# Performance work log

Hardware: AMD Instinct MI355X
Metric: run time of the kernel (lower is better)

The kernel has to match this reference:

```python
import jax, jax.numpy as jnp
import numpy as np

EPS = 1e-5

def _ln(x, g, b):
    mu = jnp.mean(x, axis=-1, keepdims=True)
    var = jnp.mean((x - mu) ** 2, axis=-1, keepdims=True)
    return (x - mu) * jax.lax.rsqrt(var + EPS) * g + b

def setup_inputs() -> dict:
    key = jax.random.key(0)
    ks = jax.random.split(key, 12)
    B, T, D, H = 8, 2048, 64, 8
    hs = D // H  # 8
    s = 0.05
    return {
        'x': jax.random.normal(ks[0], (B, T, D), dtype=jnp.float32),
        # per-head Q/K/V weights stacked: [H, hs, D] (torch Linear weight layout [out, in])
        'Wq': jax.random.normal(ks[1], (H, hs, D), dtype=jnp.float32) * s,
        'Wk': jax.random.normal(ks[2], (H, hs, D), dtype=jnp.float32) * s,
        'Wv': jax.random.normal(ks[3], (H, hs, D), dtype=jnp.float32) * s,
        'Wproj': jax.random.normal(ks[4], (D, H * hs), dtype=jnp.float32) * s,
        'bproj': jnp.zeros((D,), dtype=jnp.float32),
        'W1': jax.random.normal(ks[5], (4 * D, D), dtype=jnp.float32) * s,
        'b1': jnp.zeros((4 * D,), dtype=jnp.float32),
        'W2': jax.random.normal(ks[6], (D, 4 * D), dtype=jnp.float32) * s,
        'b2': jnp.zeros((D,), dtype=jnp.float32),
        'ln1_g': jnp.ones((D,), dtype=jnp.float32),
        'ln1_b': jnp.zeros((D,), dtype=jnp.float32),
        'ln2_g': jnp.ones((D,), dtype=jnp.float32),
        'ln2_b': jnp.zeros((D,), dtype=jnp.float32),
    }

def reference(x, Wq, Wk, Wv, Wproj, bproj, W1, b1, W2, b2, ln1_g, ln1_b, ln2_g, ln2_b):
    # pre-LN self-attention (dropout = identity, eval mode)
    h = _ln(x, ln1_g, ln1_b)
    q = jnp.einsum('btd,hsd->bhts', h, Wq)  # [B,H,T,hs]
    k = jnp.einsum('btd,hsd->bhts', h, Wk)
    v = jnp.einsum('btd,hsd->bhts', h, Wv)
    scale = Wk.shape[1] ** -0.5  # k.shape[-1]**-0.5 in original
    wei = jax.nn.softmax(jnp.einsum('bhts,bhus->bhtu', q, k) * scale, axis=-1)
    o = jnp.einsum('bhtu,bhus->bhts', wei, v)  # [B,H,T,hs]
    B, H, T, hs = o.shape
    o = o.transpose(0, 2, 1, 3).reshape(B, T, H * hs)  # concat heads
    x = x + o @ Wproj.T + bproj
    # pre-LN MLP
    h2 = _ln(x, ln2_g, ln2_b)
    ff = jax.nn.relu(h2 @ W1.T + b1) @ W2.T + b2
    return x + ff
```

## Files before the change

### kernel.cpp

```cpp
#include <hip/hip_runtime.h>
#include <hip/hip_fp16.h>

#define DEV static __device__ __forceinline__

constexpr int NTOK = 8 * 2048;
constexpr float LN_EPS = 1e-5f;

using half4  = __attribute__((ext_vector_type(4))) _Float16;
using half8  = __attribute__((ext_vector_type(8))) _Float16;
using f32x4  = __attribute__((ext_vector_type(4))) float;
using f32x16 = __attribute__((ext_vector_type(16))) float;

DEV __half2 bch2(unsigned u) { return __builtin_bit_cast(__half2, u); }
DEV unsigned bcu(__half2 h)  { return __builtin_bit_cast(unsigned, h); }

#define MFMA16(a, b, c)    __builtin_amdgcn_mfma_f32_16x16x16f16(a, b, c, 0, 0, 0)
#define MFMA32(a, b, c)    __builtin_amdgcn_mfma_f32_32x32x8f16(a, b, c, 0, 0, 0)
#define MFMA32X16(a, b, c) __builtin_amdgcn_mfma_f32_32x32x16_f16(a, b, c, 0, 0, 0)

DEV half4 pk4(float a, float b, float c, float d) {
  unsigned lo = __builtin_bit_cast(unsigned, __builtin_amdgcn_cvt_pkrtz(a, b));
  unsigned hi = __builtin_bit_cast(unsigned, __builtin_amdgcn_cvt_pkrtz(c, d));
  uint2 u = make_uint2(lo, hi);
  return __builtin_bit_cast(half4, u);
}
DEV half8 cat8(uint2 a, uint2 b) {
  uint4 u = make_uint4(a.x, a.y, b.x, b.y);
  return __builtin_bit_cast(half8, u);
}
DEV half8 cat8h(half4 a, half4 b) {
  return cat8(__builtin_bit_cast(uint2, a), __builtin_bit_cast(uint2, b));
}

DEV float schr(float x) {
  return __builtin_bit_cast(float, (int)__builtin_fmaf(x, 8388608.0f, 1064987473.0f));
}

__global__ __launch_bounds__(256) void k_ln_qkv(
    const float* __restrict__ x, const float* __restrict__ Wq,
    const float* __restrict__ Wk, const float* __restrict__ Wv,
    const float* __restrict__ g1, const float* __restrict__ b1g,
    __half* __restrict__ Qo, __half* __restrict__ Ko, __half* __restrict__ Vo)
{
  __shared__ __align__(16) __half WqF[4096];
  __shared__ __align__(16) __half WkF[4096];
  __shared__ __align__(16) __half WvF[4096];
  const int tid = threadIdx.x, lane = tid & 63, wid = tid >> 6;
  const int l15 = lane & 15, gg = lane >> 4;
  const float qs = 0.35355339059327373f * 1.4426950408889634f;
  for (int idx = tid; idx < 1024; idx += 256) {
    int mt = idx >> 8, kt = (idx >> 6) & 3, l = idx & 63;
    int row = l & 15, g = l >> 4;
    int off = (mt * 16 + row) * 64 + kt * 16 + g * 4;
    float4 a = *(const float4*)(Wq + off);
    float4 b = *(const float4*)(Wk + off);
    float4 c = *(const float4*)(Wv + off);
    half4 hq; hq[0] = (_Float16)(a.x*qs); hq[1] = (_Float16)(a.y*qs);
    hq[2] = (_Float16)(a.z*qs); hq[3] = (_Float16)(a.w*qs);
    half4 hk; hk[0] = (_Float16)b.x; hk[1] = (_Float16)b.y;
    hk[2] = (_Float16)b.z; hk[3] = (_Float16)b.w;
    half4 hv; hv[0] = (_Float16)c.x; hv[1] = (_Float16)c.y;
    hv[2] = (_Float16)c.z; hv[3] = (_Float16)c.w;
    *(half4*)&WqF[idx * 4] = hq;
    *(half4*)&WkF[idx * 4] = hk;
    *(half4*)&WvF[idx * 4] = hv;
  }
  __syncthreads();

  const int tok = (blockIdx.x * 4 + wid) * 16 + l15;
  const int b = tok >> 11, t = tok & 2047;
  float4 xv[4];
  float sum = 0.f, sq = 0.f;
  #pragma unroll
  for (int kt = 0; kt < 4; ++kt) {
    xv[kt] = *(const float4*)(x + tok * 64 + kt * 16 + gg * 4);
    sum += xv[kt].x + xv[kt].y + xv[kt].z + xv[kt].w;
    sq  += xv[kt].x*xv[kt].x + xv[kt].y*xv[kt].y
         + xv[kt].z*xv[kt].z + xv[kt].w*xv[kt].w;
  }
  sum += __shfl_xor(sum, 16); sum += __shfl_xor(sum, 32);
  sq  += __shfl_xor(sq, 16);  sq  += __shfl_xor(sq, 32);
  float mu = sum * (1.0f / 64.0f);
  float var = sq * (1.0f / 64.0f) - mu * mu;
  float rs = rsqrtf(var + LN_EPS);
  half4 hb[4];
  #pragma unroll
  for (int kt = 0; kt < 4; ++kt) {
    float4 gv = *(const float4*)(g1 + kt * 16 + gg * 4);
    float4 bv = *(const float4*)(b1g + kt * 16 + gg * 4);
    hb[kt][0] = (_Float16)((xv[kt].x - mu) * rs * gv.x + bv.x);
    hb[kt][1] = (_Float16)((xv[kt].y - mu) * rs * gv.y + bv.y);
    hb[kt][2] = (_Float16)((xv[kt].z - mu) * rs * gv.z + bv.z);
    hb[kt][3] = (_Float16)((xv[kt].w - mu) * rs * gv.w + bv.w);
  }
  #pragma unroll
  for (int mt = 0; mt < 4; ++mt) {
    f32x4 oq = {}, ok = {}, ov = {};
    #pragma unroll
    for (int kt = 0; kt < 4; ++kt) {
      half4 q_a = *(const half4*)&WqF[((mt * 4 + kt) * 64 + lane) * 4];
      half4 k_a = *(const half4*)&WkF[((mt * 4 + kt) * 64 + lane) * 4];
      half4 v_a = *(const half4*)&WvF[((mt * 4 + kt) * 64 + lane) * 4];
      oq = MFMA16(q_a, hb[kt], oq);
      ok = MFMA16(k_a, hb[kt], ok);
      ov = MFMA16(v_a, hb[kt], ov);
    }
    const int sg = mt * 16 + gg * 4;
    const int h = sg >> 3, s = sg & 7;
    const long base = ((long)(b * 8 + h) * 2048 + t) * 8 + s;
    *(half4*)(Qo + base) = pk4(oq[0], oq[1], oq[2], oq[3]);
    *(half4*)(Ko + base) = pk4(ok[0], ok[1], ok[2], ok[3]);
    *(half4*)(Vo + base) = pk4(ov[0], ov[1], ov[2], ov[3]);
  }
}

__global__ __launch_bounds__(256, 4) void k_attn(
    const __half* __restrict__ Qg, const __half* __restrict__ Kg,
    const __half* __restrict__ Vg, __half* __restrict__ Og)
{
  __shared__ __align__(16) char VTs[9 * 4128];
  const int tid = threadIdx.x, lane = tid & 63, wid = tid >> 6;
  const int bh = blockIdx.x;
  const int base = bh << 14;
  const uint4* Vu = (const uint4*)(Vg + base);
  for (int i = tid; i < 1024; i += 256) {
    uint4 a = Vu[2 * i], bq = Vu[2 * i + 1];
    const unsigned short* pa = (const unsigned short*)&a;
    const unsigned short* pb = (const unsigned short*)&bq;
    #pragma unroll
    for (int d = 0; d < 8; ++d) {
      unsigned val = (unsigned)pa[d] | ((unsigned)pb[d] << 16);
      *(unsigned*)(VTs + d * 4128 + i * 4) = val;
    }
    *(unsigned*)(VTs + 8 * 4128 + i * 4) = 0x3C003C00u;
  }
  __syncthreads();

  const int b = bh >> 3, hh = bh & 7;
  const int l31 = lane & 31, hi = lane >> 5;
  const int q0 = blockIdx.y * 256 + wid * 64;
  half4 qf0 = *(const half4*)((const char*)(Qg + base) + (q0 + l31) * 16 + hi * 8);
  half4 qf1 = *(const half4*)((const char*)(Qg + base) + (q0 + 32 + l31) * 16 + hi * 8);
  const char* kp = (const char*)(Kg + base) + l31 * 16 + hi * 8;
  const int deff = (l31 <= 8) ? l31 : 8;
  const char* vb = VTs + deff * 4128 + hi * 8;

  const f32x16 z = {};
  f32x16 o0 = {}, o1 = {};
  half4 kA[8], kB[8];
  #pragma unroll
  for (int u = 0; u < 8; ++u) kA[u] = *(const half4*)(kp + u * 512);

  #define ATTN_BODY(KF, VB, IMM)                                               \
    {                                                                          \
      f32x16 s0 = MFMA32(KF, qf0, z);                                          \
      f32x16 s1 = MFMA32(KF, qf1, z);                                          \
      uint2 vl0 = *(const uint2*)((VB) + (IMM));                               \
      uint2 vh0 = *(const uint2*)((VB) + (IMM) + 16);                          \
      uint2 vl1 = *(const uint2*)((VB) + (IMM) + 32);                          \
      uint2 vh1 = *(const uint2*)((VB) + (IMM) + 48);                          \
      half4 pa0 = pk4(schr(s0[0]),  schr(s0[1]),  schr(s0[2]),  schr(s0[3]));  \
      half4 pa1 = pk4(schr(s0[4]),  schr(s0[5]),  schr(s0[6]),  schr(s0[7]));  \
      o0 = MFMA32X16(cat8(vl0, vh0), cat8h(pa0, pa1), o0);                     \
      half4 pb0 = pk4(schr(s1[0]),  schr(s1[1]),  schr(s1[2]),  schr(s1[3]));  \
      half4 pb1 = pk4(schr(s1[4]),  schr(s1[5]),  schr(s1[6]),  schr(s1[7]));  \
      o1 = MFMA32X16(cat8(vl0, vh0), cat8h(pb0, pb1), o1);                     \
      half4 pa2 = pk4(schr(s0[8]),  schr(s0[9]),  schr(s0[10]), schr(s0[11])); \
      half4 pa3 = pk4(schr(s0[12]), schr(s0[13]), schr(s0[14]), schr(s0[15])); \
      o0 = MFMA32X16(cat8(vl1, vh1), cat8h(pa2, pa3), o0);                     \
      half4 pb2 = pk4(schr(s1[8]),  schr(s1[9]),  schr(s1[10]), schr(s1[11])); \
      half4 pb3 = pk4(schr(s1[12]), schr(s1[13]), schr(s1[14]), schr(s1[15])); \
      o1 = MFMA32X16(cat8(vl1, vh1), cat8h(pb2, pb3), o1);                     \
    }

  #pragma unroll 1
  for (int gp = 0; gp < 4; ++gp) {
    const char* vbg = vb + gp * 1024;
    const char* kpe = kp + gp * 8192;
    #pragma unroll
    for (int u = 0; u < 8; ++u) kB[u] = *(const half4*)(kpe + 4096 + u * 512);
    #pragma unroll
    for (int u = 0; u < 8; ++u) ATTN_BODY(kA[u], vbg, u * 64);
    if (gp < 3) {
      #pragma unroll
      for (int u = 0; u < 8; ++u) kA[u] = *(const half4*)(kpe + 8192 + u * 512);
    }
    #pragma unroll
    for (int u = 0; u < 8; ++u) ATTN_BODY(kB[u], vbg, 512 + u * 64);
  }
  #undef ATTN_BODY

  {
    float l0 = __shfl(o0[4], l31);
    float inv = 1.0f / l0;
    half4 r;
    r[0] = (_Float16)(o0[0] * inv); r[1] = (_Float16)(o0[1] * inv);
    r[2] = (_Float16)(o0[2] * inv); r[3] = (_Float16)(o0[3] * inv);
    *(half4*)(Og + ((b * 2048 + q0 + l31) * 64) + hh * 8 + hi * 4) = r;
  }
  {
    float l1 = __shfl(o1[4], l31);
    float inv = 1.0f / l1;
    half4 r;
    r[0] = (_Float16)(o1[0] * inv); r[1] = (_Float16)(o1[1] * inv);
    r[2] = (_Float16)(o1[2] * inv); r[3] = (_Float16)(o1[3] * inv);
    *(half4*)(Og + ((b * 2048 + q0 + 32 + l31) * 64) + hh * 8 + hi * 4) = r;
  }
}

__global__ __launch_bounds__(256) void k_proj_mlp(
    const float* __restrict__ x, const __half* __restrict__ Og,
    const float* __restrict__ Wproj, const float* __restrict__ bproj,
    const float* __restrict__ W1, const float* __restrict__ b1,
    const float* __restrict__ W2, const float* __restrict__ b2,
    const float* __restrict__ g2, const float* __restrict__ bb2,
    float* __restrict__ out)
{
  __shared__ __align__(16) __half WpF[4096];
  __shared__ __align__(16) __half W1F[16384];
  __shared__ __align__(16) __half W2F[16384];
  __shared__ __align__(16) float biasLDS[512];
  const int tid = threadIdx.x, lane = tid & 63, wid = tid >> 6;
  const int l15 = lane & 15, gg = lane >> 4;

  for (int idx = tid; idx < 1024; idx += 256) {
    int mt = idx >> 8, kt = (idx >> 6) & 3, l = idx & 63;
    int row = l & 15, g = l >> 4;
    float4 w = *(const float4*)(Wproj + (mt * 16 + row) * 64 + kt * 16 + g * 4);
    half4 h; h[0] = (_Float16)w.x; h[1] = (_Float16)w.y;
    h[2] = (_Float16)w.z; h[3] = (_Float16)w.w;
    *(half4*)&WpF[idx * 4] = h;
  }
  for (int idx = tid; idx < 4096; idx += 256) {
    int mt2 = idx >> 8, kt = (idx >> 6) & 3, l = idx & 63;
    int row = l & 15, g = l >> 4;
    float4 w = *(const float4*)(W1 + (mt2 * 16 + row) * 64 + kt * 16 + g * 4);
    half4 h; h[0] = (_Float16)w.x; h[1] = (_Float16)w.y;
    h[2] = (_Float16)w.z; h[3] = (_Float16)w.w;
    *(half4*)&W1F[idx * 4] = h;
  }
  for (int idx = tid; idx < 4096; idx += 256) {
    int mt = idx >> 10, kt2 = (idx >> 6) & 15, l = idx & 63;
    int row = l & 15, g = l >> 4;
    float4 w = *(const float4*)(W2 + (mt * 16 + row) * 256 + kt2 * 16 + g * 4);
    half4 h; h[0] = (_Float16)w.x; h[1] = (_Float16)w.y;
    h[2] = (_Float16)w.z; h[3] = (_Float16)w.w;
    *(half4*)&W2F[idx * 4] = h;
  }
  for (int idx = tid; idx < 512; idx += 256) {
    float v;
    if      (idx <  64) v = bproj[idx];
    else if (idx < 128) v = g2[idx - 64];
    else if (idx < 192) v = bb2[idx - 128];
    else if (idx < 256) v = b2[idx - 192];
    else                v = b1[idx - 256];
    biasLDS[idx] = v;
  }
  __syncthreads();

  const int tile = blockIdx.x * 4 + wid;
  const int tok = tile * 16 + l15;

  const __half* orow = Og + tok * 64;
  half4 ob[4];
  #pragma unroll
  for (int kt = 0; kt < 4; ++kt)
    ob[kt] = __builtin_bit_cast(half4, *(const uint2*)(orow + kt * 16 + gg * 4));

  f32x4 acc[4];
  #pragma unroll
  for (int mt = 0; mt < 4; ++mt) {
    float4 xv = *(const float4*)(x + tok * 64 + mt * 16 + gg * 4);
    float4 bp = *(const float4*)&biasLDS[mt * 16 + gg * 4];
    acc[mt] = (f32x4){xv.x + bp.x, xv.y + bp.y, xv.z + bp.z, xv.w + bp.w};
    #pragma unroll
    for (int kt = 0; kt < 4; ++kt) {
      half4 wa = *(const half4*)&WpF[((mt * 4 + kt) * 64 + lane) * 4];
      acc[mt] = MFMA16(wa, ob[kt], acc[mt]);
    }
  }
  float sum = 0.f, sq = 0.f;
  #pragma unroll
  for (int mt = 0; mt < 4; ++mt) {
    #pragma unroll
    for (int r = 0; r < 4; ++r) { float v = acc[mt][r]; sum += v; sq += v * v; }
  }
  sum += __shfl_xor(sum, 16); sum += __shfl_xor(sum, 32);
  sq  += __shfl_xor(sq, 16);  sq  += __shfl_xor(sq, 32);
  float mu = sum * (1.0f / 64.0f);
  float var = sq * (1.0f / 64.0f) - mu * mu;
  float rs = rsqrtf(var + LN_EPS);
  half4 hb[4];
  #pragma unroll
  for (int mt = 0; mt < 4; ++mt) {
    float4 gv = *(const float4*)&biasLDS[64 + mt * 16 + gg * 4];
    float4 bv = *(const float4*)&biasLDS[128 + mt * 16 + gg * 4];
    hb[mt][0] = (_Float16)((acc[mt][0] - mu) * rs * gv.x + bv.x);
    hb[mt][1] = (_Float16)((acc[mt][1] - mu) * rs * gv.y + bv.y);
    hb[mt][2] = (_Float16)((acc[mt][2] - mu) * rs * gv.z + bv.z);
    hb[mt][3] = (_Float16)((acc[mt][3] - mu) * rs * gv.w + bv.w);
  }
  half4 pf[16];
  #pragma unroll
  for (int mt2 = 0; mt2 < 16; ++mt2) {
    float4 b1v = *(const float4*)&biasLDS[256 + mt2 * 16 + gg * 4];
    f32x4 f = (f32x4){b1v.x, b1v.y, b1v.z, b1v.w};
    #pragma unroll
    for (int kt = 0; kt < 4; ++kt) {
      half4 wa = *(const half4*)&W1F[((mt2 * 4 + kt) * 64 + lane) * 4];
      f = MFMA16(wa, hb[kt], f);
    }
    pf[mt2][0] = (_Float16)fmaxf(f[0], 0.f);
    pf[mt2][1] = (_Float16)fmaxf(f[1], 0.f);
    pf[mt2][2] = (_Float16)fmaxf(f[2], 0.f);
    pf[mt2][3] = (_Float16)fmaxf(f[3], 0.f);
  }
  #pragma unroll
  for (int mt = 0; mt < 4; ++mt) {
    float4 b2v = *(const float4*)&biasLDS[192 + mt * 16 + gg * 4];
    f32x4 o = (f32x4){acc[mt][0] + b2v.x, acc[mt][1] + b2v.y,
                      acc[mt][2] + b2v.z, acc[mt][3] + b2v.w};
    #pragma unroll
    for (int kt2 = 0; kt2 < 16; ++kt2) {
      half4 wa = *(const half4*)&W2F[((mt * 16 + kt2) * 64 + lane) * 4];
      o = MFMA16(wa, pf[kt2], o);
    }
    *(float4*)(out + tok * 64 + mt * 16 + gg * 4) =
        make_float4(o[0], o[1], o[2], o[3]);
  }
}

extern "C" void kernel_launch(void* const* d_in, const int* in_sizes, int n_in,
                              void* d_out, int out_size, void* d_ws, size_t ws_size,
                              hipStream_t stream) {
  const float* x     = (const float*)d_in[0];
  const float* Wq    = (const float*)d_in[1];
  const float* Wk    = (const float*)d_in[2];
  const float* Wv    = (const float*)d_in[3];
  const float* Wproj = (const float*)d_in[4];
  const float* bproj = (const float*)d_in[5];
  const float* W1    = (const float*)d_in[6];
  const float* b1    = (const float*)d_in[7];
  const float* W2    = (const float*)d_in[8];
  const float* b2    = (const float*)d_in[9];
  const float* g1    = (const float*)d_in[10];
  const float* bb1   = (const float*)d_in[11];
  const float* g2    = (const float*)d_in[12];
  const float* bb2   = (const float*)d_in[13];
  float* out = (float*)d_out;

  __half* Qh = (__half*)d_ws;
  __half* Kh = Qh + 1048576;
  __half* Vh = Kh + 1048576;
  __half* Oc = Vh + 1048576;

  k_ln_qkv<<<256, 256, 0, stream>>>(x, Wq, Wk, Wv, g1, bb1, Qh, Kh, Vh);
  k_attn<<<dim3(64, 8), 256, 0, stream>>>(Qh, Kh, Vh, Oc);
  k_proj_mlp<<<256, 256, 0, stream>>>(x, Oc, Wproj, bproj, W1, b1, W2, b2,
                                      g2, bb2, out);
}
```

Baseline: 50.69 us.

## Fold Schraudolph exp scaling into weights and software-pipeline QK MFMAs

```diff
diff --git a/kernel.cpp b/kernel.cpp
--- a/kernel.cpp
+++ b/kernel.cpp
@@ -31,10 +31,7 @@
 DEV half8 cat8h(half4 a, half4 b) {
   return cat8(__builtin_bit_cast(uint2, a), __builtin_bit_cast(uint2, b));
 }
-
-DEV float schr(float x) {
-  return __builtin_bit_cast(float, (int)__builtin_fmaf(x, 8388608.0f, 1064987473.0f));
-}
+DEV float ib(float x) { return __builtin_bit_cast(float, (int)x); }
 
 __global__ __launch_bounds__(256) void k_ln_qkv(
     const float* __restrict__ x, const float* __restrict__ Wq,
@@ -47,7 +44,8 @@
   __shared__ __align__(16) __half WvF[4096];
   const int tid = threadIdx.x, lane = tid & 63, wid = tid >> 6;
   const int l15 = lane & 15, gg = lane >> 4;
-  const float qs = 0.35355339059327373f * 1.4426950408889634f;
+  const float qs = 0.35355339059327373f * 1.4426950408889634f * 2048.0f;
+  const float ks = 4096.0f;
   for (int idx = tid; idx < 1024; idx += 256) {
     int mt = idx >> 8, kt = (idx >> 6) & 3, l = idx & 63;
     int row = l & 15, g = l >> 4;
@@ -57,8 +55,8 @@
     float4 c = *(const float4*)(Wv + off);
     half4 hq; hq[0] = (_Float16)(a.x*qs); hq[1] = (_Float16)(a.y*qs);
     hq[2] = (_Float16)(a.z*qs); hq[3] = (_Float16)(a.w*qs);
-    half4 hk; hk[0] = (_Float16)b.x; hk[1] = (_Float16)b.y;
-    hk[2] = (_Float16)b.z; hk[3] = (_Float16)b.w;
+    half4 hk; hk[0] = (_Float16)(b.x*ks); hk[1] = (_Float16)(b.y*ks);
+    hk[2] = (_Float16)(b.z*ks); hk[3] = (_Float16)(b.w*ks);
     half4 hv; hv[0] = (_Float16)c.x; hv[1] = (_Float16)c.y;
     hv[2] = (_Float16)c.z; hv[3] = (_Float16)c.w;
     *(half4*)&WqF[idx * 4] = hq;
@@ -114,7 +112,7 @@
   }
 }
 
-__global__ __launch_bounds__(256, 4) void k_attn(
+__global__ __launch_bounds__(256, 2) void k_attn(
     const __half* __restrict__ Qg, const __half* __restrict__ Kg,
     const __half* __restrict__ Vg, __half* __restrict__ Og)
 {
@@ -145,33 +143,37 @@
   const int deff = (l31 <= 8) ? l31 : 8;
   const char* vb = VTs + deff * 4128 + hi * 8;
 
-  const f32x16 z = {};
-  f32x16 o0 = {}, o1 = {};
+  f32x16 cm;
+  #pragma unroll
+  for (int i = 0; i < 16; ++i) cm[i] = 1064987473.0f;
+
+  f32x16 o0l = {}, o0h = {}, o1l = {}, o1h = {};
   half4 kA[8], kB[8];
   #pragma unroll
   for (int u = 0; u < 8; ++u) kA[u] = *(const half4*)(kp + u * 512);
 
-  #define ATTN_BODY(KF, VB, IMM)                                               \
+  #define PVB(SC0, SC1, VB, IMM)                                               \
     {                                                                          \
-      f32x16 s0 = MFMA32(KF, qf0, z);                                          \
-      f32x16 s1 = MFMA32(KF, qf1, z);                                          \
       uint2 vl0 = *(const uint2*)((VB) + (IMM));                               \
       uint2 vh0 = *(const uint2*)((VB) + (IMM) + 16);                          \
       uint2 vl1 = *(const uint2*)((VB) + (IMM) + 32);                          \
       uint2 vh1 = *(const uint2*)((VB) + (IMM) + 48);                          \
-      half4 pa0 = pk4(schr(s0[0]),  schr(s0[1]),  schr(s0[2]),  schr(s0[3]));  \
-      half4 pa1 = pk4(schr(s0[4]),  schr(s0[5]),  schr(s0[6]),  schr(s0[7]));  \
-      o0 = MFMA32X16(cat8(vl0, vh0), cat8h(pa0, pa1), o0);                     \
-      half4 pb0 = pk4(schr(s1[0]),  schr(s1[1]),  schr(s1[2]),  schr(s1[3]));  \
-      half4 pb1 = pk4(schr(s1[4]),  schr(s1[5]),  schr(s1[6]),  schr(s1[7]));  \
-      o1 = MFMA32X16(cat8(vl0, vh0), cat8h(pb0, pb1), o1);                     \
-      half4 pa2 = pk4(schr(s0[8]),  schr(s0[9]),  schr(s0[10]), schr(s0[11])); \
-      half4 pa3 = pk4(schr(s0[12]), schr(s0[13]), schr(s0[14]), schr(s0[15])); \
-      o0 = MFMA32X16(cat8(vl1, vh1), cat8h(pa2, pa3), o0);                     \
-      half4 pb2 = pk4(schr(s1[8]),  schr(s1[9]),  schr(s1[10]), schr(s1[11])); \
-      half4 pb3 = pk4(schr(s1[12]), schr(s1[13]), schr(s1[14]), schr(s1[15])); \
-      o1 = MFMA32X16(cat8(vl1, vh1), cat8h(pb2, pb3), o1);                     \
-    }
+      half4 pa0 = pk4(ib(SC0[0]),  ib(SC0[1]),  ib(SC0[2]),  ib(SC0[3]));      \
+      half4 pa1 = pk4(ib(SC0[4]),  ib(SC0[5]),  ib(SC0[6]),  ib(SC0[7]));      \
+      o0l = MFMA32X16(cat8(vl0, vh0), cat8h(pa0, pa1), o0l);                   \
+      half4 pb0 = pk4(ib(SC1[0]),  ib(SC1[1]),  ib(SC1[2]),  ib(SC1[3]));      \
+      half4 pb1 = pk4(ib(SC1[4]),  ib(SC1[5]),  ib(SC1[6]),  ib(SC1[7]));      \
+      o1l = MFMA32X16(cat8(vl0, vh0), cat8h(pb0, pb1), o1l);                   \
+      half4 pa2 = pk4(ib(SC0[8]),  ib(SC0[9]),  ib(SC0[10]), ib(SC0[11]));     \
+      half4 pa3 = pk4(ib(SC0[12]), ib(SC0[13]), ib(SC0[14]), ib(SC0[15]));     \
+      o0h = MFMA32X16(cat8(vl1, vh1), cat8h(pa2, pa3), o0h);                   \
+      half4 pb2 = pk4(ib(SC1[8]),  ib(SC1[9]),  ib(SC1[10]), ib(SC1[11]));     \
+      half4 pb3 = pk4(ib(SC1[12]), ib(SC1[13]), ib(SC1[14]), ib(SC1[15]));     \
+      o1h = MFMA32X16(cat8(vl1, vh1), cat8h(pb2, pb3), o1h);                   \
+    }
+
+  f32x16 sc0 = MFMA32(kA[0], qf0, cm);
+  f32x16 sc1 = MFMA32(kA[0], qf1, cm);
 
   #pragma unroll 1
   for (int gp = 0; gp < 4; ++gp) {
@@ -180,17 +182,30 @@
     #pragma unroll
     for (int u = 0; u < 8; ++u) kB[u] = *(const half4*)(kpe + 4096 + u * 512);
     #pragma unroll
-    for (int u = 0; u < 8; ++u) ATTN_BODY(kA[u], vbg, u * 64);
+    for (int u = 0; u < 8; ++u) {
+      half4 kn = (u < 7) ? kA[u + 1] : kB[0];
+      f32x16 sn0 = MFMA32(kn, qf0, cm);
+      f32x16 sn1 = MFMA32(kn, qf1, cm);
+      PVB(sc0, sc1, vbg, u * 64);
+      sc0 = sn0; sc1 = sn1;
+    }
     if (gp < 3) {
       #pragma unroll
       for (int u = 0; u < 8; ++u) kA[u] = *(const half4*)(kpe + 8192 + u * 512);
     }
     #pragma unroll
-    for (int u = 0; u < 8; ++u) ATTN_BODY(kB[u], vbg, 512 + u * 64);
-  }
-  #undef ATTN_BODY
+    for (int u = 0; u < 8; ++u) {
+      half4 kn = (u < 7) ? kB[u + 1] : kA[0];
+      f32x16 sn0 = MFMA32(kn, qf0, cm);
+      f32x16 sn1 = MFMA32(kn, qf1, cm);
+      PVB(sc0, sc1, vbg, 512 + u * 64);
+      sc0 = sn0; sc1 = sn1;
+    }
+  }
+  #undef PVB
 
   {
+    f32x16 o0 = o0l + o0h;
     float l0 = __shfl(o0[4], l31);
     float inv = 1.0f / l0;
     half4 r;
@@ -199,6 +214,7 @@
     *(half4*)(Og + ((b * 2048 + q0 + l31) * 64) + hh * 8 + hi * 4) = r;
   }
   {
+    f32x16 o1 = o1l + o1h;
     float l1 = __shfl(o1[4], l31);
     float inv = 1.0f / l1;
     half4 r;
```

After: 46.45 us, median of 2. 1.09x faster.

## Split attention keys across two wave groups and fold the exp constant into MFMA accumulators

Applied to the files above, without the earlier changes.

```diff
diff --git a/kernel.cpp b/kernel.cpp
--- a/kernel.cpp
+++ b/kernel.cpp
@@ -31,10 +31,7 @@
 DEV half8 cat8h(half4 a, half4 b) {
   return cat8(__builtin_bit_cast(uint2, a), __builtin_bit_cast(uint2, b));
 }
-
-DEV float schr(float x) {
-  return __builtin_bit_cast(float, (int)__builtin_fmaf(x, 8388608.0f, 1064987473.0f));
-}
+DEV float ib(float x) { return __builtin_bit_cast(float, (int)x); }
 
 __global__ __launch_bounds__(256) void k_ln_qkv(
     const float* __restrict__ x, const float* __restrict__ Wq,
@@ -47,7 +44,8 @@
   __shared__ __align__(16) __half WvF[4096];
   const int tid = threadIdx.x, lane = tid & 63, wid = tid >> 6;
   const int l15 = lane & 15, gg = lane >> 4;
-  const float qs = 0.35355339059327373f * 1.4426950408889634f;
+  const float qs = 0.35355339059327373f * 1.4426950408889634f * 2048.0f;
+  const float ks = 4096.0f;
   for (int idx = tid; idx < 1024; idx += 256) {
     int mt = idx >> 8, kt = (idx >> 6) & 3, l = idx & 63;
     int row = l & 15, g = l >> 4;
@@ -57,8 +55,8 @@
     float4 c = *(const float4*)(Wv + off);
     half4 hq; hq[0] = (_Float16)(a.x*qs); hq[1] = (_Float16)(a.y*qs);
     hq[2] = (_Float16)(a.z*qs); hq[3] = (_Float16)(a.w*qs);
-    half4 hk; hk[0] = (_Float16)b.x; hk[1] = (_Float16)b.y;
-    hk[2] = (_Float16)b.z; hk[3] = (_Float16)b.w;
+    half4 hk; hk[0] = (_Float16)(b.x*ks); hk[1] = (_Float16)(b.y*ks);
+    hk[2] = (_Float16)(b.z*ks); hk[3] = (_Float16)(b.w*ks);
     half4 hv; hv[0] = (_Float16)c.x; hv[1] = (_Float16)c.y;
     hv[2] = (_Float16)c.z; hv[3] = (_Float16)c.w;
     *(half4*)&WqF[idx * 4] = hq;
@@ -114,16 +112,17 @@
   }
 }
 
-__global__ __launch_bounds__(256, 4) void k_attn(
+__global__ __launch_bounds__(512, 4) void k_attn(
     const __half* __restrict__ Qg, const __half* __restrict__ Kg,
     const __half* __restrict__ Vg, __half* __restrict__ Og)
 {
   __shared__ __align__(16) char VTs[9 * 4128];
+  __shared__ float Lc[4][2][64][5];
   const int tid = threadIdx.x, lane = tid & 63, wid = tid >> 6;
   const int bh = blockIdx.x;
   const int base = bh << 14;
   const uint4* Vu = (const uint4*)(Vg + base);
-  for (int i = tid; i < 1024; i += 256) {
+  for (int i = tid; i < 1024; i += 512) {
     uint4 a = Vu[2 * i], bq = Vu[2 * i + 1];
     const unsigned short* pa = (const unsigned short*)&a;
     const unsigned short* pb = (const unsigned short*)&bq;
@@ -138,14 +137,18 @@
 
   const int b = bh >> 3, hh = bh & 7;
   const int l31 = lane & 31, hi = lane >> 5;
-  const int q0 = blockIdx.y * 256 + wid * 64;
+  const int qt = wid & 3, kh = wid >> 2;
+  const int q0 = blockIdx.y * 256 + qt * 64;
   half4 qf0 = *(const half4*)((const char*)(Qg + base) + (q0 + l31) * 16 + hi * 8);
   half4 qf1 = *(const half4*)((const char*)(Qg + base) + (q0 + 32 + l31) * 16 + hi * 8);
-  const char* kp = (const char*)(Kg + base) + l31 * 16 + hi * 8;
+  const char* kp = (const char*)(Kg + base) + (kh << 14) + l31 * 16 + hi * 8;
   const int deff = (l31 <= 8) ? l31 : 8;
-  const char* vb = VTs + deff * 4128 + hi * 8;
-
-  const f32x16 z = {};
+  const char* vb = VTs + deff * 4128 + hi * 8 + kh * 2048;
+
+  f32x16 cm;
+  #pragma unroll
+  for (int i = 0; i < 16; ++i) cm[i] = 1064987473.0f;
+
   f32x16 o0 = {}, o1 = {};
   half4 kA[8], kB[8];
   #pragma unroll
@@ -153,35 +156,35 @@
 
   #define ATTN_BODY(KF, VB, IMM)                                               \
     {                                                                          \
-      f32x16 s0 = MFMA32(KF, qf0, z);                                          \
-      f32x16 s1 = MFMA32(KF, qf1, z);                                          \
+      f32x16 s0 = MFMA32(KF, qf0, cm);                                         \
+      f32x16 s1 = MFMA32(KF, qf1, cm);                                         \
       uint2 vl0 = *(const uint2*)((VB) + (IMM));                               \
       uint2 vh0 = *(const uint2*)((VB) + (IMM) + 16);                          \
       uint2 vl1 = *(const uint2*)((VB) + (IMM) + 32);                          \
       uint2 vh1 = *(const uint2*)((VB) + (IMM) + 48);                          \
-      half4 pa0 = pk4(schr(s0[0]),  schr(s0[1]),  schr(s0[2]),  schr(s0[3]));  \
-      half4 pa1 = pk4(schr(s0[4]),  schr(s0[5]),  schr(s0[6]),  schr(s0[7]));  \
+      half4 pa0 = pk4(ib(s0[0]),  ib(s0[1]),  ib(s0[2]),  ib(s0[3]));          \
+      half4 pa1 = pk4(ib(s0[4]),  ib(s0[5]),  ib(s0[6]),  ib(s0[7]));          \
       o0 = MFMA32X16(cat8(vl0, vh0), cat8h(pa0, pa1), o0);                     \
-      half4 pb0 = pk4(schr(s1[0]),  schr(s1[1]),  schr(s1[2]),  schr(s1[3]));  \
-      half4 pb1 = pk4(schr(s1[4]),  schr(s1[5]),  schr(s1[6]),  schr(s1[7]));  \
+      half4 pb0 = pk4(ib(s1[0]),  ib(s1[1]),  ib(s1[2]),  ib(s1[3]));          \
+      half4 pb1 = pk4(ib(s1[4]),  ib(s1[5]),  ib(s1[6]),  ib(s1[7]));          \
       o1 = MFMA32X16(cat8(vl0, vh0), cat8h(pb0, pb1), o1);                     \
-      half4 pa2 = pk4(schr(s0[8]),  schr(s0[9]),  schr(s0[10]), schr(s0[11])); \
-      half4 pa3 = pk4(schr(s0[12]), schr(s0[13]), schr(s0[14]), schr(s0[15])); \
+      half4 pa2 = pk4(ib(s0[8]),  ib(s0[9]),  ib(s0[10]), ib(s0[11]));         \
+      half4 pa3 = pk4(ib(s0[12]), ib(s0[13]), ib(s0[14]), ib(s0[15]));         \
       o0 = MFMA32X16(cat8(vl1, vh1), cat8h(pa2, pa3), o0);                     \
-      half4 pb2 = pk4(schr(s1[8]),  schr(s1[9]),  schr(s1[10]), schr(s1[11])); \
-      half4 pb3 = pk4(schr(s1[12]), schr(s1[13]), schr(s1[14]), schr(s1[15])); \
+      half4 pb2 = pk4(ib(s1[8]),  ib(s1[9]),  ib(s1[10]), ib(s1[11]));         \
+      half4 pb3 = pk4(ib(s1[12]), ib(s1[13]), ib(s1[14]), ib(s1[15]));         \
       o1 = MFMA32X16(cat8(vl1, vh1), cat8h(pb2, pb3), o1);                     \
     }
 
   #pragma unroll 1
-  for (int gp = 0; gp < 4; ++gp) {
+  for (int gp = 0; gp < 2; ++gp) {
     const char* vbg = vb + gp * 1024;
     const char* kpe = kp + gp * 8192;
     #pragma unroll
     for (int u = 0; u < 8; ++u) kB[u] = *(const half4*)(kpe + 4096 + u * 512);
     #pragma unroll
     for (int u = 0; u < 8; ++u) ATTN_BODY(kA[u], vbg, u * 64);
-    if (gp < 3) {
+    if (gp < 1) {
       #pragma unroll
       for (int u = 0; u < 8; ++u) kA[u] = *(const half4*)(kpe + 8192 + u * 512);
     }
@@ -190,21 +193,36 @@
   }
   #undef ATTN_BODY
 
-  {
-    float l0 = __shfl(o0[4], l31);
-    float inv = 1.0f / l0;
-    half4 r;
-    r[0] = (_Float16)(o0[0] * inv); r[1] = (_Float16)(o0[1] * inv);
-    r[2] = (_Float16)(o0[2] * inv); r[3] = (_Float16)(o0[3] * inv);
-    *(half4*)(Og + ((b * 2048 + q0 + l31) * 64) + hh * 8 + hi * 4) = r;
-  }
-  {
-    float l1 = __shfl(o1[4], l31);
-    float inv = 1.0f / l1;
-    half4 r;
-    r[0] = (_Float16)(o1[0] * inv); r[1] = (_Float16)(o1[1] * inv);
-    r[2] = (_Float16)(o1[2] * inv); r[3] = (_Float16)(o1[3] * inv);
-    *(half4*)(Og + ((b * 2048 + q0 + 32 + l31) * 64) + hh * 8 + hi * 4) = r;
+  if (kh) {
+    #pragma unroll
+    for (int r = 0; r < 5; ++r) {
+      Lc[qt][0][lane][r] = o0[r];
+      Lc[qt][1][lane][r] = o1[r];
+    }
+  }
+  __syncthreads();
+  if (!kh) {
+    #pragma unroll
+    for (int r = 0; r < 5; ++r) {
+      o0[r] += Lc[qt][0][lane][r];
+      o1[r] += Lc[qt][1][lane][r];
+    }
+    {
+      float l0 = __shfl(o0[4], l31);
+      float inv = 1.0f / l0;
+      half4 r;
+      r[0] = (_Float16)(o0[0] * inv); r[1] = (_Float16)(o0[1] * inv);
+      r[2] = (_Float16)(o0[2] * inv); r[3] = (_Float16)(o0[3] * inv);
+      *(half4*)(Og + ((b * 2048 + q0 + l31) * 64) + hh * 8 + hi * 4) = r;
+    }
+    {
+      float l1 = __shfl(o1[4], l31);
+      float inv = 1.0f / l1;
+      half4 r;
+      r[0] = (_Float16)(o1[0] * inv); r[1] = (_Float16)(o1[1] * inv);
+      r[2] = (_Float16)(o1[2] * inv); r[3] = (_Float16)(o1[3] * inv);
+      *(half4*)(Og + ((b * 2048 + q0 + 32 + l31) * 64) + hh * 8 + hi * 4) = r;
+    }
   }
 }
 
@@ -355,7 +373,7 @@
   __half* Oc = Vh + 1048576;
 
   k_ln_qkv<<<256, 256, 0, stream>>>(x, Wq, Wk, Wv, g1, bb1, Qh, Kh, Vh);
-  k_attn<<<dim3(64, 8), 256, 0, stream>>>(Qh, Kh, Vh, Oc);
+  k_attn<<<dim3(64, 8), 512, 0, stream>>>(Qh, Kh, Vh, Oc);
   k_proj_mlp<<<256, 256, 0, stream>>>(x, Oc, Wproj, bproj, W1, b1, W2, b2,
                                       g2, bb2, out);
 }
```

Result: slower. 59.58 us (+17.6%).
